# Performance work log

Measured on AMD Instinct MI355X. Metric: run time of the kernel, lower is better.

## Reference

```python
import jax, jax.numpy as jnp
import numpy as np
import math

FMAPS = [(80, 0.06), (40, 0.12), (20, 0.24), (10, 0.48), (5, 0.72)]
SPLITS = [0, 6400, 8000, 8400, 8500, 8525]
N_LEVELS = 5
N_CAND = 9
ALPHA_REG = 1.0   # config.reg_weights
GAMMA, F_ALPHA = 2.0, 0.25


def _make_priors():
    ps = []
    for f, s in FMAPS:
        c = (np.arange(f, dtype=np.float32) + 0.5) / f
        cy, cx = np.meshgrid(c, c, indexing="ij")
        ps.append(np.stack([cx.ravel(), cy.ravel(),
                            np.full(f * f, s, np.float32),
                            np.full(f * f, s, np.float32)], 1))
    return jnp.asarray(np.concatenate(ps, 0))


def cxcy_to_xy(b):
    return jnp.concatenate([b[..., :2] - b[..., 2:] / 2, b[..., :2] + b[..., 2:] / 2], -1)


def xy_to_cxcy(b):
    return jnp.concatenate([(b[..., :2] + b[..., 2:]) / 2, b[..., 2:] - b[..., :2]], -1)


def gcxgcy_to_cxcy(g, priors):
    cxcy = g[..., :2] * priors[..., 2:] / 10.0 + priors[..., :2]
    wh = jnp.exp(g[..., 2:] / 5.0) * priors[..., 2:]
    return jnp.concatenate([cxcy, wh], -1)


def iou_matrix(a, b):  # a [K,4] corners, b [P,4] corners -> [K,P]
    lt = jnp.maximum(a[:, None, :2], b[None, :, :2])
    rb = jnp.minimum(a[:, None, 2:], b[None, :, 2:])
    wh = jnp.clip(rb - lt, 0.0)
    inter = wh[..., 0] * wh[..., 1]
    area_a = (a[:, 2] - a[:, 0]) * (a[:, 3] - a[:, 1])
    area_b = (b[:, 2] - b[:, 0]) * (b[:, 3] - b[:, 1])
    return inter / (area_a[:, None] + area_b[None, :] - inter)


def _assign_image(boxes_i, labels_i, locs_i, priors):
    # boxes_i [K,4] xyxy, labels_i [K] int, locs_i [P,4] encoded offsets
    gt_cxcy = xy_to_cxcy(boxes_i)
    per_level, pos_ov_all = [], []
    for l in range(N_LEVELS):
        pl = priors[SPLITS[l]:SPLITS[l + 1]]                       # [Pl,4] cxcywh
        dist = jnp.linalg.norm(gt_cxcy[:, None, :2] - pl[None, :, :2], axis=-1)  # [K,Pl]
        _, top_idx = jax.lax.top_k(-dist, N_CAND)                  # [K,9] closest priors
        ov = iou_matrix(boxes_i, cxcy_to_xy(pl))                   # [K,Pl]
        pos_ov = jnp.take_along_axis(ov, top_idx, axis=1)          # [K,9]
        pos_ov_all.append(pos_ov)
        per_level.append((pl, top_idx, pos_ov, locs_i[SPLITS[l]:SPLITS[l + 1]]))
    cat = jnp.concatenate(pos_ov_all, 1)                           # [K, 5*9]
    thr = cat.mean(1) + jnp.std(cat, axis=1, ddof=1)               # torch.std is unbiased

    labels_out, gt_match, dec_match, valid_all = [], [], [], []
    for l, (pl, top_idx, pos_ov, locs_l) in enumerate(per_level):
        cand = pl[top_idx]                                          # [K,9,4]
        inside = ((boxes_i[:, None, 0] < cand[..., 0]) & (cand[..., 0] < boxes_i[:, None, 2]) &
                  (boxes_i[:, None, 1] < cand[..., 1]) & (cand[..., 1] < boxes_i[:, None, 3]))
        cand_pos = (pos_ov > thr[:, None]) & inside                 # [K,9]
        masked = jnp.where(cand_pos, pos_ov, 0.0)                   # loop init current_max_iou=0
        best_ob = jnp.argmax(masked, axis=0)                        # [9], first-max == strict-> loop
        best_iou = jnp.max(masked, axis=0)
        valid = best_iou > 0.0                                      # [9]
        lab = jnp.where(valid, labels_i[best_ob], 0)
        Pl = SPLITS[l + 1] - SPLITS[l]
        # NB: original code indexes label array by candidate index c (bug kept faithfully)
        labels_out.append(jnp.zeros(Pl, jnp.int32).at[jnp.arange(N_CAND)].set(lab))
        decoded = cxcy_to_xy(gcxgcy_to_cxcy(locs_l, pl))            # [Pl,4]
        prior_idx = top_idx[best_ob, jnp.arange(N_CAND)]            # [9]
        dec_match.append(decoded[prior_idx])
        gt_match.append(boxes_i[best_ob])
        valid_all.append(valid)
    return (jnp.concatenate(labels_out),                            # [P]
            jnp.concatenate(gt_match, 0),                           # [45,4]
            jnp.concatenate(dec_match, 0),                          # [45,4]
            jnp.concatenate(valid_all))                             # [45]


def _ciou(pred, gt):  # corner boxes [N,4]
    w1, h1 = pred[:, 2] - pred[:, 0], pred[:, 3] - pred[:, 1]
    w2, h2 = gt[:, 2] - gt[:, 0], gt[:, 3] - gt[:, 1]
    lt = jnp.maximum(pred[:, :2], gt[:, :2]); rb = jnp.minimum(pred[:, 2:], gt[:, 2:])
    wh = jnp.clip(rb - lt, 0.0)
    inter = wh[:, 0] * wh[:, 1]
    union = w1 * h1 + w2 * h2 - inter
    iou = inter / union
    c1 = (pred[:, :2] + pred[:, 2:]) / 2; c2 = (gt[:, :2] + gt[:, 2:]) / 2
    rho2 = jnp.sum((c1 - c2) ** 2, -1)
    clt = jnp.minimum(pred[:, :2], gt[:, :2]); crb = jnp.maximum(pred[:, 2:], gt[:, 2:])
    cdiag = jnp.sum((crb - clt) ** 2, -1)
    v = (4.0 / math.pi ** 2) * (jnp.arctan(w2 / h2) - jnp.arctan(w1 / h1)) ** 2
    alpha = jax.lax.stop_gradient(v / (1.0 - iou + v))
    return jnp.clip(iou - rho2 / cdiag - alpha * v, -1.0, 1.0)


def _focal(logits, targets):  # logits [N,C], targets [N] in {0..C}, 0=background
    C = logits.shape[-1]
    cls = jnp.arange(1, C + 1)
    t = targets[:, None]
    p = jax.nn.sigmoid(logits)
    term1 = (1.0 - p) ** GAMMA * jax.nn.log_sigmoid(logits)
    term2 = p ** GAMMA * jax.nn.log_sigmoid(-logits)
    pos = (t == cls).astype(logits.dtype)
    neg = ((t != cls) & (t >= 0)).astype(logits.dtype)
    return -jnp.sum(pos * F_ALPHA * term1 + neg * (1.0 - F_ALPHA) * term2)


def setup_inputs():
    key = jax.random.key(0)
    k1, k2, k3, k4, k5 = jax.random.split(key, 5)
    B, K, C, P = 32, 16, 80, 8525
    lo = jax.random.uniform(k1, (B, K, 2), minval=0.05, maxval=0.55)
    sz = jax.random.uniform(k2, (B, K, 2), minval=0.08, maxval=0.35)
    boxes = jnp.concatenate([lo, lo + sz], -1)
    labels = jax.random.randint(k3, (B, K), 1, C + 1, dtype=jnp.int32)
    predicted_locs = jax.random.normal(k4, (B, P, 4), jnp.float32)
    predicted_scores = jax.random.normal(k5, (B, P, C), jnp.float32)
    return {"predicted_locs": predicted_locs, "predicted_scores": predicted_scores,
            "boxes": boxes, "labels": labels, "priors_cxcy": _make_priors()}


def reference(predicted_locs, predicted_scores, boxes, labels, priors_cxcy):
    tc, gt_m, dec_m, valid = jax.vmap(_assign_image, in_axes=(0, 0, 0, None))(
        boxes, labels, predicted_locs, priors_cxcy)
    tc_flat = tc.reshape(-1)
    n_pos = jnp.sum(tc_flat > 0).astype(jnp.float32)
    conf_loss = _focal(predicted_scores.reshape(-1, predicted_scores.shape[-1]), tc_flat) / n_pos
    ci = _ciou(dec_m.reshape(-1, 4), gt_m.reshape(-1, 4))
    vm = valid.reshape(-1).astype(jnp.float32)
    loc_loss = jnp.sum((1.0 - ci) * vm) / jnp.maximum(vm.sum(), 1.0)
    return conf_loss + ALPHA_REG * loc_loss
```

## Files before the change

kernel.cpp:

```cpp
#include <hip/hip_runtime.h>
#include <math.h>

#define KGT   16
#define NCAND 9
#define NLVL  5
#define NPRI  8525
#define NCLS  80
#define NIMG  32

#define FOCAL_BLOCKS 2016
#define TOTAL_BLOCKS (FOCAL_BLOCKS + NIMG)
#define NELEM (NIMG * NPRI * NCLS)
#define N4    (NELEM / 4)
#define CHUNK 2707

#define OFF_IMG 8192

__device__ __forceinline__ float focal_elem(float x)
{
    float e  = __expf(-fabsf(x));
    float t  = 1.f + e;
    float r  = __builtin_amdgcn_rcpf(t);
    float sp = fmaxf(x, 0.f) + __logf(t);
    float nm = (x >= 0.f) ? 1.f : e;
    float p  = nm * r;
    return p * p * sp;
}

__device__ __forceinline__ float focal4(float4 v)
{
    return focal_elem(v.x) + focal_elem(v.y) + focal_elem(v.z) + focal_elem(v.w);
}

__global__ __launch_bounds__(256)
void atss_main(const float* __restrict__ locs,
               const float* __restrict__ scores,
               const float* __restrict__ boxes,
               const int*   __restrict__ labels,
               const float* __restrict__ priors,
               float* __restrict__ partials,
               float* __restrict__ imgstats)
{
    const int tid = threadIdx.x;
    const int blk = blockIdx.x;

    __shared__ float wsum[4];
    __shared__ float pov[KGT * 45];
    __shared__ int   tix[KGT * 45];
    __shared__ float sbox[KGT][4];
    __shared__ int   slab[KGT];
    __shared__ float thr[KGT];
    __shared__ float rc, rl;
    __shared__ int   rn;

    if (blk < FOCAL_BLOCKS) {
        const float4* s4 = (const float4*)scores;
        const int cbase = blk * CHUNK;
        bool  vld[11];
        float4 buf[11];
        #pragma unroll
        for (int k = 0; k < 8; ++k) {
            int i = cbase + k * 256 + tid;
            vld[k] = i < N4;
            buf[k] = s4[vld[k] ? i : cbase];
        }
        float a0 = 0.f, a1 = 0.f, a2 = 0.f, a3 = 0.f;
        #pragma unroll
        for (int k = 8; k < 11; ++k) {
            int i = cbase + k * 256 + tid;
            vld[k] = (k * 256 + tid < CHUNK) && (i < N4);
            buf[k] = s4[vld[k] ? i : cbase];
        }
        #pragma unroll
        for (int k = 0; k < 11; ++k) {
            float tv = focal4(buf[k]);
            float z  = vld[k] ? tv : 0.f;
            if ((k & 3) == 0) a0 += z;
            else if ((k & 3) == 1) a1 += z;
            else if ((k & 3) == 2) a2 += z;
            else a3 += z;
        }
        float lsum = (a0 + a1) + (a2 + a3);
        #pragma unroll
        for (int off = 32; off > 0; off >>= 1) lsum += __shfl_down(lsum, off);
        if ((tid & 63) == 0) wsum[tid >> 6] = lsum;
        __syncthreads();
        if (tid == 0)
            partials[blk] = wsum[0] + wsum[1] + wsum[2] + wsum[3];
        return;
    }

    const int b = blk - FOCAL_BLOCKS;
    const int SPLc[6] = {0, 6400, 8000, 8400, 8500, 8525};
    const int FDIM[5] = {80, 40, 20, 10, 5};

    if (tid == 0) { rc = 0.f; rl = 0.f; rn = 0; }
    if (tid < KGT) {
        float4 bxv = ((const float4*)boxes)[b * KGT + tid];
        sbox[tid][0] = bxv.x; sbox[tid][1] = bxv.y;
        sbox[tid][2] = bxv.z; sbox[tid][3] = bxv.w;
        slab[tid] = labels[b * KGT + tid];
    }
    __syncthreads();

    if (tid < KGT * NLVL) {
        const int g = tid / NLVL;
        const int l = tid % NLVL;
        const int f    = FDIM[l];
        const int base = SPLc[l];
        const float gcx = (sbox[g][0] + sbox[g][2]) * 0.5f;
        const float gcy = (sbox[g][1] + sbox[g][3]) * 0.5f;

        const float ff = (float)f;
        int ix0 = (int)floorf(gcx * ff); ix0 = min(max(ix0, 0), f - 1);
        int iy0 = (int)floorf(gcy * ff); iy0 = min(max(iy0, 0), f - 1);
        int sx = min(max(ix0 - 2, 0), f - 5);
        int sy = min(max(iy0 - 2, 0), f - 5);

        unsigned long long L[NCAND];
        #pragma unroll
        for (int s = 0; s < NCAND; ++s) L[s] = ~0ull;

        for (int dy = 0; dy < 5; ++dy) {
            for (int dx = 0; dx < 5; ++dx) {
                int idx = (sy + dy) * f + (sx + dx);
                float2 pc = ((const float2*)priors)[(base + idx) * 2];
                float ddx = gcx - pc.x, ddy = gcy - pc.y;
                float dist = sqrtf(ddx * ddx + ddy * ddy);
                unsigned long long pk =
                    ((unsigned long long)__float_as_uint(dist) << 32) | (unsigned)idx;
                if (pk < L[NCAND - 1]) {
                    L[NCAND - 1] = pk;
                    #pragma unroll
                    for (int s = NCAND - 1; s >= 1; --s) {
                        if (L[s] < L[s - 1]) {
                            unsigned long long tw = L[s]; L[s] = L[s - 1]; L[s - 1] = tw;
                        } else break;
                    }
                }
            }
        }
        #pragma unroll
        for (int s = 0; s < NCAND; ++s) {
            int idx = (int)(unsigned)(L[s] & 0xffffffffull);
            float4 pr = ((const float4*)priors)[base + idx];
            float px0 = pr.x - pr.z * 0.5f, py0 = pr.y - pr.w * 0.5f;
            float px1 = pr.x + pr.z * 0.5f, py1 = pr.y + pr.w * 0.5f;
            float iw = fmaxf(fminf(sbox[g][2], px1) - fmaxf(sbox[g][0], px0), 0.f);
            float ih = fmaxf(fminf(sbox[g][3], py1) - fmaxf(sbox[g][1], py0), 0.f);
            float inter = iw * ih;
            float areaA = (sbox[g][2] - sbox[g][0]) * (sbox[g][3] - sbox[g][1]);
            float areaP = (px1 - px0) * (py1 - py0);
            int o = g * 45 + l * NCAND + s;
            pov[o] = inter / (areaA + areaP - inter);
            tix[o] = idx;
        }
    }
    __syncthreads();

    if (tid < KGT) {
        float s = 0.f;
        for (int q = 0; q < 45; ++q) s += pov[tid * 45 + q];
        float mean = s / 45.f;
        float ss = 0.f;
        for (int q = 0; q < 45; ++q) { float d = pov[tid * 45 + q] - mean; ss += d * d; }
        thr[tid] = mean + sqrtf(ss / 44.f);
    }
    __syncthreads();

    if (tid < NLVL * NCAND) {
        int l = tid / NCAND, j = tid % NCAND;
        float bestv = -1.f; int bestg = 0;
        #pragma unroll
        for (int gg = 0; gg < KGT; ++gg) {
            float m = pov[gg * 45 + tid];
            int pi = tix[gg * 45 + tid];
            float4 pr = ((const float4*)priors)[SPLc[l] + pi];
            bool inside = (sbox[gg][0] < pr.x) && (pr.x < sbox[gg][2]) &&
                          (sbox[gg][1] < pr.y) && (pr.y < sbox[gg][3]);
            float mm = ((m > thr[gg]) && inside) ? m : 0.f;
            if (mm > bestv) { bestv = mm; bestg = gg; }
        }
        if (bestv > 0.f) {
            int lab = slab[bestg];
            long pos = (long)b * NPRI + SPLc[l] + j;
            float x  = scores[pos * NCLS + (lab - 1)];
            float e  = expf(-fabsf(x));
            float l1 = log1pf(e);
            float spp = fmaxf(x, 0.f) + l1;
            float spn = fmaxf(-x, 0.f) + l1;
            float p   = (x >= 0.f) ? 1.f / (1.f + e) : e / (1.f + e);
            float corr = 0.25f * (1.f - p) * (1.f - p) * spn - 0.75f * p * p * spp;

            int pi = tix[bestg * 45 + tid];
            float4 pr = ((const float4*)priors)[SPLc[l] + pi];
            float4 lc = ((const float4*)locs)[b * NPRI + SPLc[l] + pi];
            float cx = lc.x * pr.z / 10.f + pr.x;
            float cy = lc.y * pr.w / 10.f + pr.y;
            float w  = expf(lc.z / 5.f) * pr.z;
            float h  = expf(lc.w / 5.f) * pr.w;
            float qx0 = cx - w * 0.5f, qy0 = cy - h * 0.5f;
            float qx1 = cx + w * 0.5f, qy1 = cy + h * 0.5f;
            float gx0 = sbox[bestg][0], gy0 = sbox[bestg][1];
            float gx1 = sbox[bestg][2], gy1 = sbox[bestg][3];
            float w1 = qx1 - qx0, h1 = qy1 - qy0, w2 = gx1 - gx0, h2 = gy1 - gy0;
            float iw = fmaxf(fminf(qx1, gx1) - fmaxf(qx0, gx0), 0.f);
            float ih = fmaxf(fminf(qy1, gy1) - fmaxf(qy0, gy0), 0.f);
            float inter = iw * ih;
            float iou = inter / (w1 * h1 + w2 * h2 - inter);
            float dcx = (qx0 + qx1) * 0.5f - (gx0 + gx1) * 0.5f;
            float dcy = (qy0 + qy1) * 0.5f - (gy0 + gy1) * 0.5f;
            float rho2 = dcx * dcx + dcy * dcy;
            float ex = fmaxf(qx1, gx1) - fminf(qx0, gx0);
            float ey = fmaxf(qy1, gy1) - fminf(qy0, gy0);
            float cdiag = ex * ex + ey * ey;
            float da = atanf(w2 / h2) - atanf(w1 / h1);
            float v  = 0.4052847345693511f * da * da;
            float alpha = v / (1.f - iou + v);
            float ci = iou - rho2 / cdiag - alpha * v;
            ci = fminf(fmaxf(ci, -1.f), 1.f);

            atomicAdd(&rc, corr);
            atomicAdd(&rl, 1.f - ci);
            atomicAdd(&rn, 1);
        }
    }
    __syncthreads();
    if (tid == 0) {
        imgstats[b * 3 + 0] = rc;
        imgstats[b * 3 + 1] = rl;
        imgstats[b * 3 + 2] = (float)rn;
    }
}

__global__ __launch_bounds__(256)
void atss_finalize(const float* __restrict__ partials,
                   const float* __restrict__ imgstats,
                   float* __restrict__ out)
{
    const int tid = threadIdx.x;
    __shared__ float wsum[4];
    float lsum = 0.f;
    for (int i = tid; i < FOCAL_BLOCKS; i += 256) lsum += partials[i];
    #pragma unroll
    for (int off = 32; off > 0; off >>= 1) lsum += __shfl_down(lsum, off);
    if ((tid & 63) == 0) wsum[tid >> 6] = lsum;
    __syncthreads();
    if (tid == 0) {
        float base = 0.75f * (wsum[0] + wsum[1] + wsum[2] + wsum[3]);
        float corr = 0.f, loc = 0.f, cnt = 0.f;
        for (int b = 0; b < NIMG; ++b) {
            corr += imgstats[b * 3 + 0];
            loc  += imgstats[b * 3 + 1];
            cnt  += imgstats[b * 3 + 2];
        }
        float conf = (base + corr) / cnt;
        float locl = loc / fmaxf(cnt, 1.f);
        out[0] = conf + locl;
    }
}

extern "C" void kernel_launch(void* const* d_in, const int* in_sizes, int n_in,
                              void* d_out, int out_size, void* d_ws, size_t ws_size,
                              hipStream_t stream)
{
    const float* locs   = (const float*)d_in[0];
    const float* scores = (const float*)d_in[1];
    const float* boxes  = (const float*)d_in[2];
    const int*   labels = (const int*)d_in[3];
    const float* priors = (const float*)d_in[4];
    float* out = (float*)d_out;

    float* partials = (float*)d_ws;
    float* imgstats = (float*)((char*)d_ws + OFF_IMG);

    atss_main<<<TOTAL_BLOCKS, 256, 0, stream>>>(locs, scores, boxes, labels,
                                                priors, partials, imgstats);
    atss_finalize<<<1, 256, 0, stream>>>(partials, imgstats, out);
}
```

Baseline: 158.4 us.

## Stream focal-loss score loads through LDS with a triple-buffered global_load_lds pipeline

Replaces the register-held 11-deep batch of float4 score loads in the focal blocks with direct global-to-LDS loads (global_load_lds, 16 bytes) into a 3-slot ring, waiting on the vmcnt counter before each round and issuing the next load ahead. This cuts register pressure and is meant to keep loads in flight while computing. The assignment-path shared arrays are moved into the same LDS arena to keep total LDS usage down. Risks include a hand-coded waitcnt encoding that must match the outstanding load count, an extra LDS round trip per element, and fewer loads in flight than the original 11.

```diff
diff --git a/kernel.cpp b/kernel.cpp
--- a/kernel.cpp
+++ b/kernel.cpp
@@ -13,6 +13,7 @@
 #define NELEM (NIMG * NPRI * NCLS)
 #define N4    (NELEM / 4)
 #define CHUNK 2707
+#define NROUND 11
 
 #define OFF_IMG 8192
 
@@ -44,43 +45,43 @@
     const int tid = threadIdx.x;
     const int blk = blockIdx.x;
 
+    __shared__ float4 stage[3][256];
     __shared__ float wsum[4];
-    __shared__ float pov[KGT * 45];
-    __shared__ int   tix[KGT * 45];
-    __shared__ float sbox[KGT][4];
-    __shared__ int   slab[KGT];
-    __shared__ float thr[KGT];
     __shared__ float rc, rl;
     __shared__ int   rn;
 
     if (blk < FOCAL_BLOCKS) {
         const float4* s4 = (const float4*)scores;
         const int cbase = blk * CHUNK;
-        bool  vld[11];
-        float4 buf[11];
-        #pragma unroll
-        for (int k = 0; k < 8; ++k) {
-            int i = cbase + k * 256 + tid;
-            vld[k] = i < N4;
-            buf[k] = s4[vld[k] ? i : cbase];
-        }
-        float a0 = 0.f, a1 = 0.f, a2 = 0.f, a3 = 0.f;
-        #pragma unroll
-        for (int k = 8; k < 11; ++k) {
-            int i = cbase + k * 256 + tid;
-            vld[k] = (k * 256 + tid < CHUNK) && (i < N4);
-            buf[k] = s4[vld[k] ? i : cbase];
-        }
-        #pragma unroll
-        for (int k = 0; k < 11; ++k) {
-            float tv = focal4(buf[k]);
-            float z  = vld[k] ? tv : 0.f;
-            if ((k & 3) == 0) a0 += z;
-            else if ((k & 3) == 1) a1 += z;
-            else if ((k & 3) == 2) a2 += z;
-            else a3 += z;
-        }
-        float lsum = (a0 + a1) + (a2 + a3);
+        const int w = tid >> 6, lane = tid & 63;
+        const int wslice = w << 6;
+
+        #define ISSUE(k)                                                            \
+            do {                                                                    \
+                int gi_ = min(cbase + (k) * 256 + wslice + lane, N4 - 1);           \
+                __builtin_amdgcn_global_load_lds(                                   \
+                    (const __attribute__((address_space(1))) void*)(s4 + gi_),      \
+                    (__attribute__((address_space(3))) void*)&stage[(k) % 3][wslice],\
+                    16, 0, 0);                                                      \
+            } while (0)
+
+        ISSUE(0); ISSUE(1); ISSUE(2);
+
+        float a0 = 0.f, a1 = 0.f;
+        #pragma unroll
+        for (int k = 0; k < NROUND; ++k) {
+            __builtin_amdgcn_s_waitcnt(0x0F72);
+            float4 v = stage[k % 3][wslice + lane];
+            __asm__ volatile("" ::: "memory");
+            if (k + 3 < NROUND) ISSUE(k + 3);
+            bool vld = (k * 256 + tid < CHUNK) && (cbase + k * 256 + tid < N4);
+            float tv = focal4(v);
+            if (k & 1) a1 += vld ? tv : 0.f;
+            else       a0 += vld ? tv : 0.f;
+        }
+        #undef ISSUE
+
+        float lsum = a0 + a1;
         #pragma unroll
         for (int off = 32; off > 0; off >>= 1) lsum += __shfl_down(lsum, off);
         if ((tid & 63) == 0) wsum[tid >> 6] = lsum;
@@ -94,11 +95,18 @@
     const int SPLc[6] = {0, 6400, 8000, 8400, 8500, 8525};
     const int FDIM[5] = {80, 40, 20, 10, 5};
 
+    float* arena = (float*)stage;
+    float* pov  = arena;
+    int*   tix  = (int*)(arena + 720);
+    float* sbox = arena + 1440;
+    int*   slab = (int*)(arena + 1504);
+    float* thr  = arena + 1520;
+
     if (tid == 0) { rc = 0.f; rl = 0.f; rn = 0; }
     if (tid < KGT) {
         float4 bxv = ((const float4*)boxes)[b * KGT + tid];
-        sbox[tid][0] = bxv.x; sbox[tid][1] = bxv.y;
-        sbox[tid][2] = bxv.z; sbox[tid][3] = bxv.w;
+        sbox[tid * 4 + 0] = bxv.x; sbox[tid * 4 + 1] = bxv.y;
+        sbox[tid * 4 + 2] = bxv.z; sbox[tid * 4 + 3] = bxv.w;
         slab[tid] = labels[b * KGT + tid];
     }
     __syncthreads();
@@ -108,8 +116,8 @@
         const int l = tid % NLVL;
         const int f    = FDIM[l];
         const int base = SPLc[l];
-        const float gcx = (sbox[g][0] + sbox[g][2]) * 0.5f;
-        const float gcy = (sbox[g][1] + sbox[g][3]) * 0.5f;
+        const float gcx = (sbox[g * 4 + 0] + sbox[g * 4 + 2]) * 0.5f;
+        const float gcy = (sbox[g * 4 + 1] + sbox[g * 4 + 3]) * 0.5f;
 
         const float ff = (float)f;
         int ix0 = (int)floorf(gcx * ff); ix0 = min(max(ix0, 0), f - 1);
@@ -146,10 +154,10 @@
             float4 pr = ((const float4*)priors)[base + idx];
             float px0 = pr.x - pr.z * 0.5f, py0 = pr.y - pr.w * 0.5f;
             float px1 = pr.x + pr.z * 0.5f, py1 = pr.y + pr.w * 0.5f;
-            float iw = fmaxf(fminf(sbox[g][2], px1) - fmaxf(sbox[g][0], px0), 0.f);
-            float ih = fmaxf(fminf(sbox[g][3], py1) - fmaxf(sbox[g][1], py0), 0.f);
+            float iw = fmaxf(fminf(sbox[g*4+2], px1) - fmaxf(sbox[g*4+0], px0), 0.f);
+            float ih = fmaxf(fminf(sbox[g*4+3], py1) - fmaxf(sbox[g*4+1], py0), 0.f);
             float inter = iw * ih;
-            float areaA = (sbox[g][2] - sbox[g][0]) * (sbox[g][3] - sbox[g][1]);
+            float areaA = (sbox[g*4+2] - sbox[g*4+0]) * (sbox[g*4+3] - sbox[g*4+1]);
             float areaP = (px1 - px0) * (py1 - py0);
             int o = g * 45 + l * NCAND + s;
             pov[o] = inter / (areaA + areaP - inter);
@@ -176,8 +184,8 @@
             float m = pov[gg * 45 + tid];
             int pi = tix[gg * 45 + tid];
             float4 pr = ((const float4*)priors)[SPLc[l] + pi];
-            bool inside = (sbox[gg][0] < pr.x) && (pr.x < sbox[gg][2]) &&
-                          (sbox[gg][1] < pr.y) && (pr.y < sbox[gg][3]);
+            bool inside = (sbox[gg*4+0] < pr.x) && (pr.x < sbox[gg*4+2]) &&
+                          (sbox[gg*4+1] < pr.y) && (pr.y < sbox[gg*4+3]);
             float mm = ((m > thr[gg]) && inside) ? m : 0.f;
             if (mm > bestv) { bestv = mm; bestg = gg; }
         }
@@ -201,8 +209,8 @@
             float h  = expf(lc.w / 5.f) * pr.w;
             float qx0 = cx - w * 0.5f, qy0 = cy - h * 0.5f;
             float qx1 = cx + w * 0.5f, qy1 = cy + h * 0.5f;
-            float gx0 = sbox[bestg][0], gy0 = sbox[bestg][1];
-            float gx1 = sbox[bestg][2], gy1 = sbox[bestg][3];
+            float gx0 = sbox[bestg*4+0], gy0 = sbox[bestg*4+1];
+            float gx1 = sbox[bestg*4+2], gy1 = sbox[bestg*4+3];
             float w1 = qx1 - qx0, h1 = qy1 - qy0, w2 = gx1 - gx0, h2 = gy1 - gy0;
             float iw = fmaxf(fminf(qx1, gx1) - fmaxf(qx0, gx0), 0.f);
             float ih = fmaxf(fminf(qy1, gy1) - fmaxf(qy0, gy0), 0.f);
```

After: 161.7 us. 1.02x slower.
